# Kernel optimization log

Hardware: AMD Instinct MI355X
Metric: run time of the kernel (lower is better)

## Reference

```python
import jax, jax.numpy as jnp
import numpy as np
import math

S, B, D, H = 2048, 2, 1024, 16
DK = D // H


def setup_inputs() -> dict:
    key = jax.random.key(0)
    ks = jax.random.split(key, 13)
    scale = 1.0 / math.sqrt(D)
    inp = {
        "query": jax.random.normal(ks[0], (S, B, D), jnp.float32),
        "key": jax.random.normal(ks[1], (S, B, D), jnp.float32),
        "value": jax.random.normal(ks[2], (S, B, D), jnp.float32),
        "mask": jax.random.normal(ks[3], (B, S, S), jnp.float32),
        # four Linear(d_model, d_model) layers: q, k, v, out. torch convention W:(out,in)
        "Wq": jax.random.normal(ks[4], (D, D), jnp.float32) * scale,
        "bq": jax.random.normal(ks[5], (D,), jnp.float32) * scale,
        "Wk": jax.random.normal(ks[6], (D, D), jnp.float32) * scale,
        "bk": jax.random.normal(ks[7], (D,), jnp.float32) * scale,
        "Wv": jax.random.normal(ks[8], (D, D), jnp.float32) * scale,
        "bv": jax.random.normal(ks[9], (D,), jnp.float32) * scale,
        "Wo": jax.random.normal(ks[10], (D, D), jnp.float32) * scale,
        "bo": jax.random.normal(ks[11], (D,), jnp.float32) * scale,
    }
    return inp


def reference(query, key, value, mask, Wq, bq, Wk, bk, Wv, bv, Wo, bo):
    # inputs are (tokens S, batch B, d_model D)
    def proj(x, W, b):  # torch Linear: x @ W.T + b, then split heads -> (B,H,S,DK)
        y = jnp.einsum('sbd,ed->sbe', x, W) + b
        return y.reshape(S, B, H, DK).transpose(1, 2, 0, 3)

    q = proj(query, Wq, bq)
    k = proj(key, Wk, bk)
    v = proj(value, Wv, bv)

    scores = jnp.einsum('bhsd,bhtd->bhst', q, k) / math.sqrt(DK)
    scores = scores + mask[:, None, :, :]  # broadcast over heads
    p_attn = jax.nn.softmax(scores, axis=-1)  # (B,H,S,S)

    x = jnp.einsum('bhst,bhtd->bhsd', p_attn, v)  # (B,H,S,DK)
    x = x.transpose(2, 0, 1, 3).reshape(S, B, D)  # (S,B,D)
    out = jnp.einsum('sbd,ed->sbe', x, Wo) + bo

    attn = p_attn.mean(axis=1)  # mean over heads -> (B,S,S)
    return out, attn
```

## Files before the change

kernel.cpp:

```cpp
#include <hip/hip_runtime.h>
#include <hip/hip_bf16.h>


#define S_LEN 2048
#define BATCH 2
#define DMODEL 1024
#define NH 16
#define DKH 64
#define SCALE 0.125f
#define QSCALE 0.180336878f
#define FMAX 20.0f
#define KSTRIDE 72

typedef __bf16 bf16_t;
typedef __attribute__((ext_vector_type(8))) __bf16 bf16x8;
typedef __attribute__((ext_vector_type(8))) unsigned short u16x8;
typedef __attribute__((ext_vector_type(4))) unsigned short u16x4;
typedef __attribute__((ext_vector_type(4))) float f32x4;

__device__ __forceinline__ unsigned short f32_bf16_rne(float f) {
  union { float f; unsigned int u; } v; v.f = f;
  unsigned int u = v.u;
  u += 0x7fffu + ((u >> 16) & 1u);
  return (unsigned short)(u >> 16);
}
__device__ __forceinline__ float bf16u_f32(unsigned short us) {
  union { unsigned int u; float f; } v; v.u = ((unsigned int)us) << 16;
  return v.f;
}
__device__ __forceinline__ f32x4 mfma_bf16(bf16x8 a, bf16x8 b, f32x4 c) {
  return __builtin_amdgcn_mfma_f32_16x16x32_bf16(a, b, c, 0, 0, 0);
}
__device__ __forceinline__ float exp2_fast(float x) {
#if __has_builtin(__builtin_amdgcn_exp2f)
  return __builtin_amdgcn_exp2f(x);
#else
  return __expf(x * 0.69314718f);
#endif
}
__device__ __forceinline__ unsigned int cvtpk(float lo, float hi) {
  unsigned int r;
  asm("v_cvt_pk_bf16_f32 %0, %1, %2" : "=v"(r) : "v"(lo), "v"(hi));
  return r;
}
__device__ __forceinline__ void gload16(const bf16_t* g, unsigned short* l) {
  __builtin_amdgcn_global_load_lds(
      (const __attribute__((address_space(1))) void*)g,
      (__attribute__((address_space(3))) void*)l, 16, 0, 0);
}

__global__ __launch_bounds__(256) void cvt_w_kernel(
    const float* __restrict__ w0, const float* __restrict__ w1,
    const float* __restrict__ w2, const float* __restrict__ w3,
    bf16_t* __restrict__ o0, bf16_t* __restrict__ o1,
    bf16_t* __restrict__ o2, bf16_t* __restrict__ o3) {
  const float* src; bf16_t* dst;
  switch (blockIdx.y) {
    case 0: src = w0; dst = o0; break;
    case 1: src = w1; dst = o1; break;
    case 2: src = w2; dst = o2; break;
    default: src = w3; dst = o3; break;
  }
  int i = (blockIdx.x * 256 + threadIdx.x) * 4;
  float4 v = *(const float4*)(src + i);
  union { unsigned short u[4]; uint2 q; } r;
  r.u[0] = f32_bf16_rne(v.x); r.u[1] = f32_bf16_rne(v.y);
  r.u[2] = f32_bf16_rne(v.z); r.u[3] = f32_bf16_rne(v.w);
  *(uint2*)(dst + i) = r.q;
}

__global__ __launch_bounds__(256) void cvt_x_kernel(
    const float* __restrict__ x0, const float* __restrict__ x1,
    const float* __restrict__ x2,
    bf16_t* __restrict__ o0, bf16_t* __restrict__ o1, bf16_t* __restrict__ o2) {
  const float* src; bf16_t* dst;
  switch (blockIdx.y) {
    case 0: src = x0; dst = o0; break;
    case 1: src = x1; dst = o1; break;
    default: src = x2; dst = o2; break;
  }
  int i = (blockIdx.x * 256 + threadIdx.x) * 4;
  float4 v = *(const float4*)(src + i);
  union { unsigned short u[4]; uint2 q; } r;
  r.u[0] = f32_bf16_rne(v.x); r.u[1] = f32_bf16_rne(v.y);
  r.u[2] = f32_bf16_rne(v.z); r.u[3] = f32_bf16_rne(v.w);
  *(uint2*)(dst + i) = r.q;
}

__global__ __launch_bounds__(256) void cvt_mask_kernel(
    const float* __restrict__ m, bf16_t* __restrict__ o) {
  int i = (blockIdx.x * 256 + threadIdx.x) * 4;
  float4 v = *(const float4*)(m + i);
  union { unsigned short u[4]; uint2 q; } r;
  r.u[0] = f32_bf16_rne(__expf(v.x - FMAX));
  r.u[1] = f32_bf16_rne(__expf(v.y - FMAX));
  r.u[2] = f32_bf16_rne(__expf(v.z - FMAX));
  r.u[3] = f32_bf16_rne(__expf(v.w - FMAX));
  *(uint2*)(o + i) = r.q;
}

__global__ __launch_bounds__(256) void proj_kernel(
    const bf16_t* __restrict__ Xq, const bf16_t* __restrict__ Xk, const bf16_t* __restrict__ Xv,
    const bf16_t* __restrict__ Wqb, const bf16_t* __restrict__ Wkb, const bf16_t* __restrict__ Wvb,
    const float* __restrict__ bq, const float* __restrict__ bk, const float* __restrict__ bv,
    bf16_t* __restrict__ qo, bf16_t* __restrict__ ko, bf16_t* __restrict__ vTo) {
  int mode = blockIdx.z;
  const bf16_t* X = (mode == 0) ? Xq : (mode == 1) ? Xk : Xv;
  const bf16_t* W = (mode == 0) ? Wqb : (mode == 1) ? Wkb : Wvb;
  const float* bias = (mode == 0) ? bq : (mode == 1) ? bk : bv;

  __shared__ __align__(16) unsigned short Alds[128 * 32];
  __shared__ __align__(16) unsigned short Blds[128 * 32];

  int tid = threadIdx.x;
  int wv = tid >> 6, lane = tid & 63, quad = lane >> 4, col = lane & 15;
  int wr = wv >> 1, wc = wv & 1;
  int rowbase = blockIdx.x * 128;
  int colbase = blockIdx.y * 128;

  int srow = tid >> 2;
  int sk8 = (tid & 3) * 8;
  const bf16_t* ga0 = X + (size_t)(rowbase + srow) * DMODEL + sk8;
  const bf16_t* gb0 = W + (size_t)(colbase + srow) * DMODEL + sk8;
  unsigned short* la0 = Alds + tid * 8;
  unsigned short* lb0 = Blds + tid * 8;

  f32x4 acc[4][4] = {};

  for (int k0 = 0; k0 < DMODEL; k0 += 32) {
    gload16(ga0 + k0, la0);
    gload16(ga0 + 64 * DMODEL + k0, la0 + 2048);
    gload16(gb0 + k0, lb0);
    gload16(gb0 + 64 * DMODEL + k0, lb0 + 2048);
    __syncthreads();

    union { u16x8 u; bf16x8 v; } af[4], bfr[4];
#pragma unroll
    for (int mi = 0; mi < 4; ++mi)
      af[mi].u = *(const u16x8*)(Alds + (wr * 64 + mi * 16 + col) * 32 + quad * 8);
#pragma unroll
    for (int ni = 0; ni < 4; ++ni)
      bfr[ni].u = *(const u16x8*)(Blds + (wc * 64 + ni * 16 + col) * 32 + quad * 8);
#pragma unroll
    for (int mi = 0; mi < 4; ++mi)
#pragma unroll
      for (int ni = 0; ni < 4; ++ni)
        acc[mi][ni] = mfma_bf16(af[mi].v, bfr[ni].v, acc[mi][ni]);
    __syncthreads();
  }

  float biasv[4];
#pragma unroll
  for (int ni = 0; ni < 4; ++ni)
    biasv[ni] = bias[colbase + wc * 64 + ni * 16 + col];

#pragma unroll
  for (int mi = 0; mi < 4; ++mi)
#pragma unroll
    for (int ni = 0; ni < 4; ++ni)
#pragma unroll
      for (int r = 0; r < 4; ++r) {
        int grow = rowbase + wr * 64 + mi * 16 + quad * 4 + r;
        int gcol = colbase + wc * 64 + ni * 16 + col;
        float val = acc[mi][ni][r] + biasv[ni];
        if (mode == 0) val *= QSCALE;
        unsigned short us = f32_bf16_rne(val);
        int s = grow >> 1, bb = grow & 1;
        int h = gcol >> 6, dk = gcol & 63;
        if (mode == 2) {
          ((unsigned short*)vTo)[((size_t)(bb * NH + h) * DKH + dk) * S_LEN + s] = us;
        } else {
          unsigned short* dst = (unsigned short*)(mode == 0 ? qo : ko);
          dst[((size_t)(bb * NH + h) * S_LEN + s) * DKH + dk] = us;
        }
      }
}

__global__ __launch_bounds__(256) void flash_kernel(
    const bf16_t* __restrict__ emb,
    const bf16_t* __restrict__ q_ws, const bf16_t* __restrict__ k_ws,
    const bf16_t* __restrict__ vT_ws,
    bf16_t* __restrict__ x_ws, float* __restrict__ rl_ws) {
  int tid = threadIdx.x;
  int w = tid >> 6, lane = tid & 63, quad = lane >> 4, col = lane & 15;

  int bid = blockIdx.x;
  int wi = bid >> 3;
  int bh = (bid & 7) * 4 + (wi & 3);
  int qblk = wi >> 2;
  int b = bh >> 4;
  int s0 = qblk * 128 + w * 32;
  int sA = s0, sB = s0 + 16;

  __shared__ __align__(16) unsigned short Klds[64 * KSTRIDE];
  __shared__ __align__(16) unsigned short Vlds[64 * KSTRIDE];

  const bf16_t* qh = q_ws + (size_t)bh * S_LEN * DKH;
  const bf16_t* kh = k_ws + (size_t)bh * S_LEN * DKH;
  const bf16_t* vh = vT_ws + (size_t)bh * DKH * S_LEN;
  const unsigned short* emA = (const unsigned short*)emb +
      (size_t)b * S_LEN * S_LEN + (size_t)(sA + col) * S_LEN;
  const unsigned short* emB = emA + (size_t)16 * S_LEN;

  bf16x8 qA0 = *(const bf16x8*)(qh + (sA + col) * DKH + quad * 8);
  bf16x8 qA1 = *(const bf16x8*)(qh + (sA + col) * DKH + 32 + quad * 8);
  bf16x8 qB0 = *(const bf16x8*)(qh + (sB + col) * DKH + quad * 8);
  bf16x8 qB1 = *(const bf16x8*)(qh + (sB + col) * DKH + 32 + quad * 8);

  int row1 = tid >> 3, row2 = row1 + 32;
  int ch = (tid & 7) * 8;
  int pi1 = (row1 & 32) + ((row1 & 16) >> 2) + ((row1 & 12) << 1) + (row1 & 3);
  int pi2 = (row2 & 32) + ((row2 & 16) >> 2) + ((row2 & 12) << 1) + (row2 & 3);
  const unsigned short* kg1 = (const unsigned short*)kh + (size_t)pi1 * DKH + ch;
  const unsigned short* kg2 = (const unsigned short*)kh + (size_t)pi2 * DKH + ch;
  const unsigned short* vg1 = (const unsigned short*)vh + (size_t)row1 * S_LEN + ch;
  const unsigned short* vg2 = (const unsigned short*)vh + (size_t)row2 * S_LEN + ch;
  u16x8* kl1 = (u16x8*)(Klds + row1 * KSTRIDE + ch);
  u16x8* kl2 = (u16x8*)(Klds + row2 * KSTRIDE + ch);
  u16x8* vl1 = (u16x8*)(Vlds + row1 * KSTRIDE + ch);
  u16x8* vl2 = (u16x8*)(Vlds + row2 * KSTRIDE + ch);

  f32x4 xA[4] = {}, xB[4] = {};
  float lsumA = 0.0f, lsumB = 0.0f;

  u16x8 kp1 = *(const u16x8*)kg1;
  u16x8 kp2 = *(const u16x8*)kg2;
  u16x8 vp1 = *(const u16x8*)vg1;
  u16x8 vp2 = *(const u16x8*)vg2;

  for (int t0 = 0; t0 < S_LEN; t0 += 64) {
    *kl1 = kp1; *kl2 = kp2; *vl1 = vp1; *vl2 = vp2;
    __syncthreads();

    if (t0 + 64 < S_LEN) {
      kp1 = *(const u16x8*)(kg1 + (size_t)(t0 + 64) * DKH);
      kp2 = *(const u16x8*)(kg2 + (size_t)(t0 + 64) * DKH);
      vp1 = *(const u16x8*)(vg1 + (t0 + 64));
      vp2 = *(const u16x8*)(vg2 + (t0 + 64));
    }

    u16x4 emA4[4], emB4[4];
#pragma unroll
    for (int j = 0; j < 4; ++j) {
      int f = t0 + ((j >> 1) << 5) + ((j & 1) << 2) + quad * 8;
      emA4[j] = *(const u16x4*)(emA + f);
      emB4[j] = *(const u16x4*)(emB + f);
    }

    f32x4 CA[4], CB[4];
#pragma unroll
    for (int j = 0; j < 4; ++j) {
      union { u16x8 u; bf16x8 v; } kb0, kb1;
      int row = j * 16 + col;
      kb0.u = *(const u16x8*)(Klds + row * KSTRIDE + quad * 8);
      kb1.u = *(const u16x8*)(Klds + row * KSTRIDE + 32 + quad * 8);
      f32x4 z = {};
      CA[j] = mfma_bf16(kb1.v, qA1, mfma_bf16(kb0.v, qA0, z));
      CB[j] = mfma_bf16(kb1.v, qB1, mfma_bf16(kb0.v, qB0, z));
    }

    unsigned int PA[8], PB[8];
#pragma unroll
    for (int j = 0; j < 4; ++j) {
      float a0 = exp2_fast(CA[j][0]) * bf16u_f32(emA4[j][0]);
      float a1 = exp2_fast(CA[j][1]) * bf16u_f32(emA4[j][1]);
      float a2 = exp2_fast(CA[j][2]) * bf16u_f32(emA4[j][2]);
      float a3 = exp2_fast(CA[j][3]) * bf16u_f32(emA4[j][3]);
      lsumA += (a0 + a1) + (a2 + a3);
      PA[j * 2] = cvtpk(a0, a1);
      PA[j * 2 + 1] = cvtpk(a2, a3);
      float b0 = exp2_fast(CB[j][0]) * bf16u_f32(emB4[j][0]);
      float b1 = exp2_fast(CB[j][1]) * bf16u_f32(emB4[j][1]);
      float b2 = exp2_fast(CB[j][2]) * bf16u_f32(emB4[j][2]);
      float b3 = exp2_fast(CB[j][3]) * bf16u_f32(emB4[j][3]);
      lsumB += (b0 + b1) + (b2 + b3);
      PB[j * 2] = cvtpk(b0, b1);
      PB[j * 2 + 1] = cvtpk(b2, b3);
    }
    union { unsigned int u32[4]; bf16x8 v; } bA0, bA1, bB0, bB1;
#pragma unroll
    for (int i = 0; i < 4; ++i) {
      bA0.u32[i] = PA[i]; bA1.u32[i] = PA[4 + i];
      bB0.u32[i] = PB[i]; bB1.u32[i] = PB[4 + i];
    }

#pragma unroll
    for (int ni = 0; ni < 4; ++ni) {
      union { u16x8 u; bf16x8 v; } vb0, vb1;
      int row = ni * 16 + col;
      vb0.u = *(const u16x8*)(Vlds + row * KSTRIDE + quad * 8);
      vb1.u = *(const u16x8*)(Vlds + row * KSTRIDE + 32 + quad * 8);
      xA[ni] = mfma_bf16(vb1.v, bA1.v, mfma_bf16(vb0.v, bA0.v, xA[ni]));
      xB[ni] = mfma_bf16(vb1.v, bB1.v, mfma_bf16(vb0.v, bB0.v, xB[ni]));
    }
    __syncthreads();
  }

  lsumA += __shfl_xor(lsumA, 16, 64); lsumA += __shfl_xor(lsumA, 32, 64);
  lsumB += __shfl_xor(lsumB, 16, 64); lsumB += __shfl_xor(lsumB, 32, 64);
  float rlA = 1.0f / lsumA, rlB = 1.0f / lsumB;

  unsigned short* xo = (unsigned short*)x_ws;
#pragma unroll
  for (int ni = 0; ni < 4; ++ni) {
    uint2 wa, wb;
    wa.x = cvtpk(xA[ni][0] * rlA, xA[ni][1] * rlA);
    wa.y = cvtpk(xA[ni][2] * rlA, xA[ni][3] * rlA);
    wb.x = cvtpk(xB[ni][0] * rlB, xB[ni][1] * rlB);
    wb.y = cvtpk(xB[ni][2] * rlB, xB[ni][3] * rlB);
    *(uint2*)(xo + ((size_t)bh * S_LEN + sA + col) * DKH + ni * 16 + quad * 4) = wa;
    *(uint2*)(xo + ((size_t)bh * S_LEN + sB + col) * DKH + ni * 16 + quad * 4) = wb;
  }
  if (quad == 0) {
    rl_ws[(size_t)bh * S_LEN + sA + col] = rlA;
    rl_ws[(size_t)bh * S_LEN + sB + col] = rlB;
  }
}

__global__ __launch_bounds__(256) void attn_kernel(
    const bf16_t* __restrict__ emb,
    const bf16_t* __restrict__ q_ws, const bf16_t* __restrict__ k_ws,
    const float* __restrict__ rl_ws,
    float* __restrict__ attn_out) {
  int tid = threadIdx.x;
  int w = tid >> 6, lane = tid & 63, quad = lane >> 4, col = lane & 15;
  int b = blockIdx.y;
  int s0 = blockIdx.x * 64 + w * 16;
  int t_base = blockIdx.z * 128;

  __shared__ __align__(16) unsigned short Klds[128 * KSTRIDE];

  const unsigned short* emrow = (const unsigned short*)emb +
      (size_t)b * S_LEN * S_LEN + (size_t)(s0 + quad * 4) * S_LEN + t_base;
  float emf[8][4];
  for (int j = 0; j < 8; ++j)
    for (int r = 0; r < 4; ++r)
      emf[j][r] = bf16u_f32(emrow[r * S_LEN + j * 16 + col]);

  f32x4 acc[8] = {};

  int srow_a = w * 8 + (lane >> 3), schunk_a = (lane & 7) * 8;
  const bf16_t* kh0 = k_ws + (size_t)(b * NH) * S_LEN * DKH;

  u16x8 kpre[4];
#pragma unroll
  for (int i = 0; i < 4; ++i)
    kpre[i] = *(const u16x8*)(kh0 + (size_t)(t_base + i * 32 + srow_a) * DKH + schunk_a);

  for (int h = 0; h < NH; ++h) {
    int bh = b * NH + h;
    const bf16_t* qh = q_ws + (size_t)bh * S_LEN * DKH;

#pragma unroll
    for (int i = 0; i < 4; ++i)
      *(u16x8*)(Klds + (i * 32 + srow_a) * KSTRIDE + schunk_a) = kpre[i];
    __syncthreads();

    if (h + 1 < NH) {
      const bf16_t* khn = kh0 + (size_t)(h + 1) * S_LEN * DKH;
#pragma unroll
      for (int i = 0; i < 4; ++i)
        kpre[i] = *(const u16x8*)(khn + (size_t)(t_base + i * 32 + srow_a) * DKH + schunk_a);
    }

    bf16x8 qf0 = *(const bf16x8*)(qh + (s0 + col) * DKH + quad * 8);
    bf16x8 qf1 = *(const bf16x8*)(qh + (s0 + col) * DKH + 32 + quad * 8);
    float rl4[4];
    for (int r = 0; r < 4; ++r) rl4[r] = rl_ws[bh * S_LEN + s0 + quad * 4 + r];

#pragma unroll
    for (int j = 0; j < 8; ++j) {
      int row = j * 16 + col;
      union { u16x8 u; bf16x8 v; } kb0, kb1;
      kb0.u = *(const u16x8*)(Klds + row * KSTRIDE + quad * 8);
      kb1.u = *(const u16x8*)(Klds + row * KSTRIDE + 32 + quad * 8);
      f32x4 z = {};
      f32x4 C = mfma_bf16(qf1, kb1.v, mfma_bf16(qf0, kb0.v, z));
#pragma unroll
      for (int r = 0; r < 4; ++r) {
        float t = exp2_fast(C[r]) * emf[j][r];
        acc[j][r] = fmaf(t, rl4[r], acc[j][r]);
      }
    }
    __syncthreads();
  }

  for (int j = 0; j < 8; ++j)
    for (int r = 0; r < 4; ++r)
      attn_out[((size_t)b * S_LEN + s0 + quad * 4 + r) * S_LEN + t_base + j * 16 + col] =
          acc[j][r] * (1.0f / NH);
}

__global__ __launch_bounds__(256) void outproj_kernel(
    const bf16_t* __restrict__ x_ws, const bf16_t* __restrict__ Wob,
    const float* __restrict__ bo, float* __restrict__ out) {
  __shared__ __align__(16) unsigned short Alds[128 * 32];
  __shared__ __align__(16) unsigned short Blds[128 * 32];

  int tid = threadIdx.x;
  int wv = tid >> 6, lane = tid & 63, quad = lane >> 4, col = lane & 15;
  int wr = wv >> 1, wc = wv & 1;
  int rowbase = blockIdx.x * 128;
  int colbase = blockIdx.y * 128;

  int srow = tid >> 2;
  int sk8 = (tid & 3) * 8;
  int r0 = rowbase + srow;
  int s0a = r0 >> 1, b0a = r0 & 1;
  int r1 = r0 + 64;
  int s1a = r1 >> 1, b1a = r1 & 1;
  const bf16_t* gb0 = Wob + (size_t)(colbase + srow) * DMODEL + sk8;
  unsigned short* la0 = Alds + tid * 8;
  unsigned short* lb0 = Blds + tid * 8;

  f32x4 acc[4][4] = {};

  for (int k0 = 0; k0 < DMODEL; k0 += 32) {
    int h = k0 >> 6, dk = (k0 & 63) + sk8;
    gload16(x_ws + ((size_t)(b0a * NH + h) * S_LEN + s0a) * DKH + dk, la0);
    gload16(x_ws + ((size_t)(b1a * NH + h) * S_LEN + s1a) * DKH + dk, la0 + 2048);
    gload16(gb0 + k0, lb0);
    gload16(gb0 + 64 * DMODEL + k0, lb0 + 2048);
    __syncthreads();

    union { u16x8 u; bf16x8 v; } af[4], bfr[4];
#pragma unroll
    for (int mi = 0; mi < 4; ++mi)
      af[mi].u = *(const u16x8*)(Alds + (wr * 64 + mi * 16 + col) * 32 + quad * 8);
#pragma unroll
    for (int ni = 0; ni < 4; ++ni)
      bfr[ni].u = *(const u16x8*)(Blds + (wc * 64 + ni * 16 + col) * 32 + quad * 8);
#pragma unroll
    for (int mi = 0; mi < 4; ++mi)
#pragma unroll
      for (int ni = 0; ni < 4; ++ni)
        acc[mi][ni] = mfma_bf16(af[mi].v, bfr[ni].v, acc[mi][ni]);
    __syncthreads();
  }

  float biasv[4];
#pragma unroll
  for (int ni = 0; ni < 4; ++ni)
    biasv[ni] = bo[colbase + wc * 64 + ni * 16 + col];

#pragma unroll
  for (int mi = 0; mi < 4; ++mi)
#pragma unroll
    for (int ni = 0; ni < 4; ++ni)
#pragma unroll
      for (int r = 0; r < 4; ++r) {
        int grow = rowbase + wr * 64 + mi * 16 + quad * 4 + r;
        int gcol = colbase + wc * 64 + ni * 16 + col;
        out[(size_t)grow * DMODEL + gcol] = acc[mi][ni][r] + biasv[ni];
      }
}

extern "C" void kernel_launch(void* const* d_in, const int* in_sizes, int n_in,
                              void* d_out, int out_size, void* d_ws, size_t ws_size,
                              hipStream_t stream) {
  const float* query = (const float*)d_in[0];
  const float* key_  = (const float*)d_in[1];
  const float* value = (const float*)d_in[2];
  const float* mask  = (const float*)d_in[3];
  const float* Wq = (const float*)d_in[4];
  const float* bq = (const float*)d_in[5];
  const float* Wk = (const float*)d_in[6];
  const float* bk = (const float*)d_in[7];
  const float* Wv = (const float*)d_in[8];
  const float* bv = (const float*)d_in[9];
  const float* Wo = (const float*)d_in[10];
  const float* bo = (const float*)d_in[11];

  char* ws = (char*)d_ws;
  bf16_t* q_ws  = (bf16_t*)(ws + 0);
  bf16_t* k_ws  = (bf16_t*)(ws + 8388608);
  bf16_t* vT_ws = (bf16_t*)(ws + 16777216);
  bf16_t* x_ws  = (bf16_t*)(ws + 25165824);
  float*  rl_ws = (float*)(ws + 33554432);
  bf16_t* Wqb = (bf16_t*)(ws + 33816576);
  bf16_t* Wkb = (bf16_t*)(ws + 35913728);
  bf16_t* Wvb = (bf16_t*)(ws + 38010880);
  bf16_t* Wob = (bf16_t*)(ws + 40108032);
  bf16_t* Xq_b = x_ws;
  bf16_t* Xk_b = (bf16_t*)(ws + 42205184);
  bf16_t* Xv_b = (bf16_t*)(ws + 50593792);
  bf16_t* emb  = (bf16_t*)(ws + 42205184);

  float* outp  = (float*)d_out;
  float* attnp = outp + (size_t)S_LEN * BATCH * DMODEL;

  cvt_w_kernel<<<dim3(1024, 4), 256, 0, stream>>>(Wq, Wk, Wv, Wo, Wqb, Wkb, Wvb, Wob);
  cvt_x_kernel<<<dim3(4096, 3), 256, 0, stream>>>(query, key_, value, Xq_b, Xk_b, Xv_b);
  proj_kernel<<<dim3(32, 8, 3), 256, 0, stream>>>(Xq_b, Xk_b, Xv_b,
                                                  Wqb, Wkb, Wvb, bq, bk, bv,
                                                  q_ws, k_ws, vT_ws);
  cvt_mask_kernel<<<dim3(8192), 256, 0, stream>>>(mask, emb);
  flash_kernel<<<dim3(512), 256, 0, stream>>>(emb, q_ws, k_ws, vT_ws, x_ws, rl_ws);
  attn_kernel<<<dim3(32, 2, 16), 256, 0, stream>>>(emb, q_ws, k_ws, rl_ws, attnp);
  outproj_kernel<<<dim3(32, 8), 256, 0, stream>>>(x_ws, Wob, bo, outp);
}
```

Measured before the change: 338.9 us.

## Load K fragments directly from global memory and factor mask exp out of head loop

The attention-probability kernel no longer stages K tiles through LDS with __syncthreads and register prefetch. Each wave now reads its K fragments straight from global (L1/L2-cached) memory. The per-element multiply by exp(mask) is factored out of the head loop and applied once at the final store, since it does not depend on the head. This removes barriers and LDS traffic and saves one multiply per element per head. The cost is redundant global loads of K across the four waves and less latency hiding.

```diff
diff --git a/kernel.cpp b/kernel.cpp
--- a/kernel.cpp
+++ b/kernel.cpp
@@ -328,67 +328,50 @@
   int s0 = blockIdx.x * 64 + w * 16;
   int t_base = blockIdx.z * 128;
 
-  __shared__ __align__(16) unsigned short Klds[128 * KSTRIDE];
-
   const unsigned short* emrow = (const unsigned short*)emb +
       (size_t)b * S_LEN * S_LEN + (size_t)(s0 + quad * 4) * S_LEN + t_base;
   float emf[8][4];
+#pragma unroll
   for (int j = 0; j < 8; ++j)
+#pragma unroll
     for (int r = 0; r < 4; ++r)
       emf[j][r] = bf16u_f32(emrow[r * S_LEN + j * 16 + col]);
 
   f32x4 acc[8] = {};
 
-  int srow_a = w * 8 + (lane >> 3), schunk_a = (lane & 7) * 8;
-  const bf16_t* kh0 = k_ws + (size_t)(b * NH) * S_LEN * DKH;
-
-  u16x8 kpre[4];
-#pragma unroll
-  for (int i = 0; i < 4; ++i)
-    kpre[i] = *(const u16x8*)(kh0 + (size_t)(t_base + i * 32 + srow_a) * DKH + schunk_a);
+  const bf16_t* qh0 = q_ws + (size_t)(b * NH) * S_LEN * DKH + (size_t)(s0 + col) * DKH;
+  const bf16_t* kh0 = k_ws + (size_t)(b * NH) * S_LEN * DKH + (size_t)(t_base + col) * DKH;
+  const float* rlp = rl_ws + (size_t)(b * NH) * S_LEN + s0 + quad * 4;
 
   for (int h = 0; h < NH; ++h) {
-    int bh = b * NH + h;
-    const bf16_t* qh = q_ws + (size_t)bh * S_LEN * DKH;
-
-#pragma unroll
-    for (int i = 0; i < 4; ++i)
-      *(u16x8*)(Klds + (i * 32 + srow_a) * KSTRIDE + schunk_a) = kpre[i];
-    __syncthreads();
-
-    if (h + 1 < NH) {
-      const bf16_t* khn = kh0 + (size_t)(h + 1) * S_LEN * DKH;
-#pragma unroll
-      for (int i = 0; i < 4; ++i)
-        kpre[i] = *(const u16x8*)(khn + (size_t)(t_base + i * 32 + srow_a) * DKH + schunk_a);
-    }
-
-    bf16x8 qf0 = *(const bf16x8*)(qh + (s0 + col) * DKH + quad * 8);
-    bf16x8 qf1 = *(const bf16x8*)(qh + (s0 + col) * DKH + 32 + quad * 8);
+    const bf16_t* qp = qh0 + (size_t)h * S_LEN * DKH;
+    bf16x8 qf0 = *(const bf16x8*)(qp + quad * 8);
+    bf16x8 qf1 = *(const bf16x8*)(qp + 32 + quad * 8);
+    const float* rlh = rlp + (size_t)h * S_LEN;
     float rl4[4];
-    for (int r = 0; r < 4; ++r) rl4[r] = rl_ws[bh * S_LEN + s0 + quad * 4 + r];
-
+#pragma unroll
+    for (int r = 0; r < 4; ++r) rl4[r] = rlh[r];
+
+    const bf16_t* kt = kh0 + (size_t)h * S_LEN * DKH;
 #pragma unroll
     for (int j = 0; j < 8; ++j) {
-      int row = j * 16 + col;
-      union { u16x8 u; bf16x8 v; } kb0, kb1;
-      kb0.u = *(const u16x8*)(Klds + row * KSTRIDE + quad * 8);
-      kb1.u = *(const u16x8*)(Klds + row * KSTRIDE + 32 + quad * 8);
+      const bf16_t* kr = kt + (size_t)(j * 16) * DKH;
+      bf16x8 kb0 = *(const bf16x8*)(kr + quad * 8);
+      bf16x8 kb1 = *(const bf16x8*)(kr + 32 + quad * 8);
       f32x4 z = {};
-      f32x4 C = mfma_bf16(qf1, kb1.v, mfma_bf16(qf0, kb0.v, z));
-#pragma unroll
-      for (int r = 0; r < 4; ++r) {
-        float t = exp2_fast(C[r]) * emf[j][r];
-        acc[j][r] = fmaf(t, rl4[r], acc[j][r]);
-      }
-    }
-    __syncthreads();
-  }
-
+      f32x4 C = mfma_bf16(qf1, kb1, mfma_bf16(qf0, kb0, z));
+#pragma unroll
+      for (int r = 0; r < 4; ++r)
+        acc[j][r] = fmaf(exp2_fast(C[r]), rl4[r], acc[j][r]);
+    }
+  }
+
+#pragma unroll
   for (int j = 0; j < 8; ++j)
+#pragma unroll
     for (int r = 0; r < 4; ++r)
       attn_out[((size_t)b * S_LEN + s0 + quad * 4 + r) * S_LEN + t_base + j * 16 + col] =
-          acc[j][r] * (1.0f / NH);
+          acc[j][r] * emf[j][r] * (1.0f / NH);
 }
 
 __global__ __launch_bounds__(256) void outproj_kernel(
```

New measurement: 410.9 us. +21.2%, slower.
